# Kernel optimization log

Hardware: AMD Instinct MI355X
Metric: run time of the kernel (lower is better)

## Reference

```python
import jax, jax.numpy as jnp
import numpy as np

K = 3          # kernel_size (hardcoded in forward)
D = 1          # dilation (hardcoded in forward)
ALPHA_3 = 1.0  # self.alpha_3
THRESH = 0.1   # self.vetorch_thresh


def unfold_wo_center(x):
    """x: (B, C, H, W) -> neighbors (B, C, K*K-1, H, W), center excluded.
    Matches F.unfold(kernel=K, dilation=D, padding same) reshaped to
    (B, C, K*K, H, W) with the center tap (index K*K//2) removed.
    Implemented as shifted views of the zero-padded input (no im2col blowup
    beyond the necessary K*K-1 copies)."""
    B, C, H, W = x.shape
    pad = (K + (D - 1) * (K - 1)) // 2
    xp = jnp.pad(x, ((0, 0), (0, 0), (pad, pad), (pad, pad)))
    offs = [(i * D, j * D) for i in range(K) for j in range(K)]
    del offs[(K * K) // 2]  # drop center -> 8 neighbors for K=3
    nbrs = jnp.stack([xp[:, :, oy:oy + H, ox:ox + W] for oy, ox in offs], axis=2)
    return nbrs  # (B, C, 8, H, W)


def _neighbor_norm(x):
    # ||x_p - x_q||_2 over channel dim -> (B, 8, H, W)
    diff = x[:, :, None] - unfold_wo_center(x)
    return jnp.sqrt(jnp.sum(diff * diff, axis=1))


def setup_inputs() -> dict:
    key = jax.random.key(0)
    k1, k2 = jax.random.split(key)
    return {
        "images_lab": jax.random.normal(k1, (16, 3, 256, 256), dtype=jnp.float32),
        "pixel_vector": jax.random.normal(k2, (16, 6, 256, 256), dtype=jnp.float32),
    }


def reference(images_lab, pixel_vector):
    # get_lab_neighbor_diff: exp(-alpha * ||lab diff||)
    W_ij = jnp.exp(-ALPHA_3 * _neighbor_norm(images_lab))   # (B, 8, H, W)
    # get_vector_neighbor_diff: ||embedding diff||
    vector_ij = _neighbor_norm(pixel_vector)                # (B, 8, H, W)
    # neighbor_loss = mean((W_ij >= thresh) * vector_ij)
    neighbor_loss = jnp.mean(
        (W_ij >= THRESH).astype(vector_ij.dtype) * vector_ij
    )
    sim_maps = jnp.concatenate([W_ij, vector_ij], axis=1)   # (B, 16, H, W)
    return sim_maps, neighbor_loss
```

## Files before the change

### kernel.cpp

```cpp
#include <hip/hip_runtime.h>

#define HWSZ 65536
#define OUT_MAPS (16 * 16 * HWSZ)
#define NBLK 512

typedef float fvec4 __attribute__((ext_vector_type(4)));

__device__ __forceinline__ void expand_row(fvec4 m, int lane, float v[6]) {
    float lft = __shfl_up(m.w, 1, 64);
    float rgt = __shfl_down(m.x, 1, 64);
    if (lane == 0)  lft = 0.f;
    if (lane == 63) rgt = 0.f;
    v[0] = lft; v[1] = m.x; v[2] = m.y; v[3] = m.z; v[4] = m.w; v[5] = rgt;
}

__global__ __launch_bounds__(256, 2) void sim_main(
    const float* __restrict__ lab,
    const float* __restrict__ vec,
    float* __restrict__ out,
    float* __restrict__ partials)
{
    const int bs   = ((blockIdx.x & 7) << 6) | (blockIdx.x >> 3);
    const int g    = bs * 256 + threadIdx.x;
    const int lane = threadIdx.x & 63;
    const int wv   = g >> 6;
    const int b    = wv >> 7;
    const int h0   = (wv & 127) << 1;
    const int w0   = lane << 2;

    const bool hasU = (h0 > 0);
    const bool hasD = (h0 < 254);

    constexpr int DY[8] = {-1,-1,-1, 0, 0, 1, 1, 1};
    constexpr int DX[8] = {-1, 0, 1,-1, 1,-1, 0, 1};

    const fvec4 zz = {0.f, 0.f, 0.f, 0.f};

    fvec4 L[3][4];
    fvec4 V[6][4];
    {
        const float* pl = lab + b * 3 * HWSZ + h0 * 256 + w0;
        #pragma unroll
        for (int c = 0; c < 3; ++c) {
            L[c][0] = hasU ? *reinterpret_cast<const fvec4*>(pl + c * HWSZ - 256) : zz;
            L[c][1] =        *reinterpret_cast<const fvec4*>(pl + c * HWSZ);
            L[c][2] =        *reinterpret_cast<const fvec4*>(pl + c * HWSZ + 256);
            L[c][3] = hasD ? *reinterpret_cast<const fvec4*>(pl + c * HWSZ + 512) : zz;
        }
        const float* pv = vec + b * 6 * HWSZ + h0 * 256 + w0;
        #pragma unroll
        for (int c = 0; c < 6; ++c) {
            V[c][0] = hasU ? *reinterpret_cast<const fvec4*>(pv + c * HWSZ - 256) : zz;
            V[c][1] =        *reinterpret_cast<const fvec4*>(pv + c * HWSZ);
            V[c][2] =        *reinterpret_cast<const fvec4*>(pv + c * HWSZ + 256);
            V[c][3] = hasD ? *reinterpret_cast<const fvec4*>(pv + c * HWSZ + 512) : zz;
        }
    }

    float accA[8][4], accB[8][4];
    float* ob = out + b * 16 * HWSZ + h0 * 256 + w0;

    #pragma unroll
    for (int k = 0; k < 8; ++k)
        #pragma unroll
        for (int j = 0; j < 4; ++j) { accA[k][j] = 0.f; accB[k][j] = 0.f; }

    #pragma unroll
    for (int c = 0; c < 3; ++c) {
        float v[4][6];
        #pragma unroll
        for (int r = 0; r < 4; ++r) expand_row(L[c][r], lane, v[r]);
        #pragma unroll
        for (int k = 0; k < 8; ++k) {
            const int r = DY[k] + 1, dx = DX[k];
            #pragma unroll
            for (int j = 0; j < 4; ++j) {
                const float dA = v[1][j + 1] - v[r][j + 1 + dx];
                accA[k][j] = fmaf(dA, dA, accA[k][j]);
                const float dB = v[2][j + 1] - v[r + 1][j + 1 + dx];
                accB[k][j] = fmaf(dB, dB, accB[k][j]);
            }
        }
    }

    unsigned maskA = 0, maskB = 0;
    #pragma unroll
    for (int k = 0; k < 8; ++k) {
        float wA[4], wB[4];
        #pragma unroll
        for (int j = 0; j < 4; ++j) {
            wA[j] = __expf(-__builtin_amdgcn_sqrtf(accA[k][j]));
            wB[j] = __expf(-__builtin_amdgcn_sqrtf(accB[k][j]));
            if (wA[j] >= 0.1f) maskA |= 1u << (k * 4 + j);
            if (wB[j] >= 0.1f) maskB |= 1u << (k * 4 + j);
        }
        fvec4 sA = {wA[0], wA[1], wA[2], wA[3]};
        fvec4 sB = {wB[0], wB[1], wB[2], wB[3]};
        *reinterpret_cast<fvec4*>(ob + k * HWSZ)       = sA;
        *reinterpret_cast<fvec4*>(ob + k * HWSZ + 256) = sB;
    }

    #pragma unroll
    for (int k = 0; k < 8; ++k)
        #pragma unroll
        for (int j = 0; j < 4; ++j) { accA[k][j] = 0.f; accB[k][j] = 0.f; }

    #pragma unroll
    for (int c = 0; c < 6; ++c) {
        float v[4][6];
        #pragma unroll
        for (int r = 0; r < 4; ++r) expand_row(V[c][r], lane, v[r]);
        #pragma unroll
        for (int k = 0; k < 8; ++k) {
            const int r = DY[k] + 1, dx = DX[k];
            #pragma unroll
            for (int j = 0; j < 4; ++j) {
                const float dA = v[1][j + 1] - v[r][j + 1 + dx];
                accA[k][j] = fmaf(dA, dA, accA[k][j]);
                const float dB = v[2][j + 1] - v[r + 1][j + 1 + dx];
                accB[k][j] = fmaf(dB, dB, accB[k][j]);
            }
        }
    }

    float lsum = 0.f;
    #pragma unroll
    for (int k = 0; k < 8; ++k) {
        float vA[4], vB[4];
        #pragma unroll
        for (int j = 0; j < 4; ++j) {
            vA[j] = __builtin_amdgcn_sqrtf(accA[k][j]);
            vB[j] = __builtin_amdgcn_sqrtf(accB[k][j]);
            if (maskA & (1u << (k * 4 + j))) lsum += vA[j];
            if (maskB & (1u << (k * 4 + j))) lsum += vB[j];
        }
        fvec4 sA = {vA[0], vA[1], vA[2], vA[3]};
        fvec4 sB = {vB[0], vB[1], vB[2], vB[3]};
        *reinterpret_cast<fvec4*>(ob + (8 + k) * HWSZ)       = sA;
        *reinterpret_cast<fvec4*>(ob + (8 + k) * HWSZ + 256) = sB;
    }

    #pragma unroll
    for (int off = 32; off > 0; off >>= 1)
        lsum += __shfl_down(lsum, off, 64);
    __shared__ float ws[4];
    const int wid = threadIdx.x >> 6;
    if (lane == 0) ws[wid] = lsum;
    __syncthreads();
    if (threadIdx.x == 0)
        partials[blockIdx.x] = ws[0] + ws[1] + ws[2] + ws[3];
}

__global__ __launch_bounds__(256) void loss_reduce(
    const float* __restrict__ partials, float* __restrict__ out_loss)
{
    float s = 0.f;
    #pragma unroll
    for (int i = 0; i < NBLK / 256; ++i)
        s += partials[i * 256 + threadIdx.x];
    #pragma unroll
    for (int off = 32; off > 0; off >>= 1)
        s += __shfl_down(s, off, 64);
    __shared__ float ws[4];
    const int lane = threadIdx.x & 63;
    const int wid  = threadIdx.x >> 6;
    if (lane == 0) ws[wid] = s;
    __syncthreads();
    if (threadIdx.x == 0)
        out_loss[0] = (ws[0] + ws[1] + ws[2] + ws[3]) / 8388608.0f;
}

extern "C" void kernel_launch(void* const* d_in, const int* in_sizes, int n_in,
                              void* d_out, int out_size, void* d_ws, size_t ws_size,
                              hipStream_t stream) {
    const float* lab = (const float*)d_in[0];
    const float* vec = (const float*)d_in[1];
    float* out      = (float*)d_out;
    float* partials = (float*)d_ws;

    sim_main<<<NBLK, 256, 0, stream>>>(lab, vec, out, partials);
    loss_reduce<<<1, 256, 0, stream>>>(partials, out + OUT_MAPS);
}
```

Before: 23.46 us.

## Process four rows per wave to reuse halo rows and defer loads

Each wave now produces four output rows instead of two. Its input window grows from four rows to six, so the halo overhead per output row drops (about 1.5x reads instead of 2x). Blocks shrink to 128 threads so the grid size stays the same. The last two input rows are loaded only after the first half's compute is issued, which overlaps that memory latency with ALU work. The cost is higher register pressure and half as many waves in flight, which can reduce latency hiding in a kernel that is mostly memory-bound.

```diff
diff --git a/kernel.cpp b/kernel.cpp
--- a/kernel.cpp
+++ b/kernel.cpp
@@ -14,73 +14,84 @@
     v[0] = lft; v[1] = m.x; v[2] = m.y; v[3] = m.z; v[4] = m.w; v[5] = rgt;
 }
 
-__global__ __launch_bounds__(256, 2) void sim_main(
+__device__ __forceinline__ void stencil2(const float v[4][6],
+                                         float accA[8][4], float accB[8][4]) {
+    constexpr int DY[8] = {-1,-1,-1, 0, 0, 1, 1, 1};
+    constexpr int DX[8] = {-1, 0, 1,-1, 1,-1, 0, 1};
+    #pragma unroll
+    for (int k = 0; k < 8; ++k) {
+        const int r = DY[k] + 1, dx = DX[k];
+        #pragma unroll
+        for (int j = 0; j < 4; ++j) {
+            const float dA = v[1][j + 1] - v[r][j + 1 + dx];
+            accA[k][j] = fmaf(dA, dA, accA[k][j]);
+            const float dB = v[2][j + 1] - v[r + 1][j + 1 + dx];
+            accB[k][j] = fmaf(dB, dB, accB[k][j]);
+        }
+    }
+}
+
+__global__ __launch_bounds__(128, 2) void sim_main(
     const float* __restrict__ lab,
     const float* __restrict__ vec,
     float* __restrict__ out,
     float* __restrict__ partials)
 {
     const int bs   = ((blockIdx.x & 7) << 6) | (blockIdx.x >> 3);
-    const int g    = bs * 256 + threadIdx.x;
     const int lane = threadIdx.x & 63;
-    const int wv   = g >> 6;
-    const int b    = wv >> 7;
-    const int h0   = (wv & 127) << 1;
+    const int wid  = threadIdx.x >> 6;
+    const int wv   = bs * 2 + wid;
+    const int b    = wv >> 6;
+    const int h0   = (wv & 63) << 2;
     const int w0   = lane << 2;
 
     const bool hasU = (h0 > 0);
-    const bool hasD = (h0 < 254);
-
-    constexpr int DY[8] = {-1,-1,-1, 0, 0, 1, 1, 1};
-    constexpr int DX[8] = {-1, 0, 1,-1, 1,-1, 0, 1};
+    const bool hasD = (h0 < 252);
 
     const fvec4 zz = {0.f, 0.f, 0.f, 0.f};
-
-    fvec4 L[3][4];
-    fvec4 V[6][4];
-    {
-        const float* pl = lab + b * 3 * HWSZ + h0 * 256 + w0;
-        #pragma unroll
-        for (int c = 0; c < 3; ++c) {
-            L[c][0] = hasU ? *reinterpret_cast<const fvec4*>(pl + c * HWSZ - 256) : zz;
-            L[c][1] =        *reinterpret_cast<const fvec4*>(pl + c * HWSZ);
-            L[c][2] =        *reinterpret_cast<const fvec4*>(pl + c * HWSZ + 256);
-            L[c][3] = hasD ? *reinterpret_cast<const fvec4*>(pl + c * HWSZ + 512) : zz;
-        }
-        const float* pv = vec + b * 6 * HWSZ + h0 * 256 + w0;
-        #pragma unroll
-        for (int c = 0; c < 6; ++c) {
-            V[c][0] = hasU ? *reinterpret_cast<const fvec4*>(pv + c * HWSZ - 256) : zz;
-            V[c][1] =        *reinterpret_cast<const fvec4*>(pv + c * HWSZ);
-            V[c][2] =        *reinterpret_cast<const fvec4*>(pv + c * HWSZ + 256);
-            V[c][3] = hasD ? *reinterpret_cast<const fvec4*>(pv + c * HWSZ + 512) : zz;
-        }
+    const float* pl = lab + b * 3 * HWSZ + h0 * 256 + w0;
+    const float* pv = vec + b * 6 * HWSZ + h0 * 256 + w0;
+    float* ob = out + b * 16 * HWSZ + h0 * 256 + w0;
+
+    fvec4 L0[3], L1[3], L2[3], L3[3], L4[3], L5[3];
+    fvec4 V0[6], V1[6], V2[6], V3[6], V4[6], V5[6];
+    #pragma unroll
+    for (int c = 0; c < 3; ++c) {
+        L0[c] = hasU ? *reinterpret_cast<const fvec4*>(pl + c * HWSZ - 256) : zz;
+        L1[c] =        *reinterpret_cast<const fvec4*>(pl + c * HWSZ);
+        L2[c] =        *reinterpret_cast<const fvec4*>(pl + c * HWSZ + 256);
+        L3[c] =        *reinterpret_cast<const fvec4*>(pl + c * HWSZ + 512);
+    }
+    #pragma unroll
+    for (int c = 0; c < 6; ++c) {
+        V0[c] = hasU ? *reinterpret_cast<const fvec4*>(pv + c * HWSZ - 256) : zz;
+        V1[c] =        *reinterpret_cast<const fvec4*>(pv + c * HWSZ);
+        V2[c] =        *reinterpret_cast<const fvec4*>(pv + c * HWSZ + 256);
+        V3[c] =        *reinterpret_cast<const fvec4*>(pv + c * HWSZ + 512);
     }
 
     float accA[8][4], accB[8][4];
-    float* ob = out + b * 16 * HWSZ + h0 * 256 + w0;
-
-    #pragma unroll
-    for (int k = 0; k < 8; ++k)
-        #pragma unroll
-        for (int j = 0; j < 4; ++j) { accA[k][j] = 0.f; accB[k][j] = 0.f; }
-
-    #pragma unroll
-    for (int c = 0; c < 3; ++c) {
-        float v[4][6];
-        #pragma unroll
-        for (int r = 0; r < 4; ++r) expand_row(L[c][r], lane, v[r]);
-        #pragma unroll
-        for (int k = 0; k < 8; ++k) {
-            const int r = DY[k] + 1, dx = DX[k];
-            #pragma unroll
-            for (int j = 0; j < 4; ++j) {
-                const float dA = v[1][j + 1] - v[r][j + 1 + dx];
-                accA[k][j] = fmaf(dA, dA, accA[k][j]);
-                const float dB = v[2][j + 1] - v[r + 1][j + 1 + dx];
-                accB[k][j] = fmaf(dB, dB, accB[k][j]);
-            }
-        }
+    float lsum = 0.f;
+
+    #pragma unroll
+    for (int k = 0; k < 8; ++k)
+        #pragma unroll
+        for (int j = 0; j < 4; ++j) { accA[k][j] = 0.f; accB[k][j] = 0.f; }
+
+    #pragma unroll
+    for (int c = 0; c < 3; ++c) {
+        float v[4][6];
+        expand_row(L0[c], lane, v[0]);
+        expand_row(L1[c], lane, v[1]);
+        expand_row(L2[c], lane, v[2]);
+        expand_row(L3[c], lane, v[3]);
+        stencil2(v, accA, accB);
+    }
+
+    #pragma unroll
+    for (int c = 0; c < 3; ++c) {
+        L4[c] =        *reinterpret_cast<const fvec4*>(pl + c * HWSZ + 768);
+        L5[c] = hasD ? *reinterpret_cast<const fvec4*>(pl + c * HWSZ + 1024) : zz;
     }
 
     unsigned maskA = 0, maskB = 0;
@@ -108,22 +119,19 @@
     #pragma unroll
     for (int c = 0; c < 6; ++c) {
         float v[4][6];
-        #pragma unroll
-        for (int r = 0; r < 4; ++r) expand_row(V[c][r], lane, v[r]);
-        #pragma unroll
-        for (int k = 0; k < 8; ++k) {
-            const int r = DY[k] + 1, dx = DX[k];
-            #pragma unroll
-            for (int j = 0; j < 4; ++j) {
-                const float dA = v[1][j + 1] - v[r][j + 1 + dx];
-                accA[k][j] = fmaf(dA, dA, accA[k][j]);
-                const float dB = v[2][j + 1] - v[r + 1][j + 1 + dx];
-                accB[k][j] = fmaf(dB, dB, accB[k][j]);
-            }
-        }
-    }
-
-    float lsum = 0.f;
+        expand_row(V0[c], lane, v[0]);
+        expand_row(V1[c], lane, v[1]);
+        expand_row(V2[c], lane, v[2]);
+        expand_row(V3[c], lane, v[3]);
+        stencil2(v, accA, accB);
+    }
+
+    #pragma unroll
+    for (int c = 0; c < 6; ++c) {
+        V4[c] =        *reinterpret_cast<const fvec4*>(pv + c * HWSZ + 768);
+        V5[c] = hasD ? *reinterpret_cast<const fvec4*>(pv + c * HWSZ + 1024) : zz;
+    }
+
     #pragma unroll
     for (int k = 0; k < 8; ++k) {
         float vA[4], vB[4];
@@ -141,14 +149,76 @@
     }
 
     #pragma unroll
+    for (int k = 0; k < 8; ++k)
+        #pragma unroll
+        for (int j = 0; j < 4; ++j) { accA[k][j] = 0.f; accB[k][j] = 0.f; }
+
+    #pragma unroll
+    for (int c = 0; c < 3; ++c) {
+        float v[4][6];
+        expand_row(L2[c], lane, v[0]);
+        expand_row(L3[c], lane, v[1]);
+        expand_row(L4[c], lane, v[2]);
+        expand_row(L5[c], lane, v[3]);
+        stencil2(v, accA, accB);
+    }
+
+    maskA = 0; maskB = 0;
+    #pragma unroll
+    for (int k = 0; k < 8; ++k) {
+        float wA[4], wB[4];
+        #pragma unroll
+        for (int j = 0; j < 4; ++j) {
+            wA[j] = __expf(-__builtin_amdgcn_sqrtf(accA[k][j]));
+            wB[j] = __expf(-__builtin_amdgcn_sqrtf(accB[k][j]));
+            if (wA[j] >= 0.1f) maskA |= 1u << (k * 4 + j);
+            if (wB[j] >= 0.1f) maskB |= 1u << (k * 4 + j);
+        }
+        fvec4 sA = {wA[0], wA[1], wA[2], wA[3]};
+        fvec4 sB = {wB[0], wB[1], wB[2], wB[3]};
+        *reinterpret_cast<fvec4*>(ob + k * HWSZ + 512) = sA;
+        *reinterpret_cast<fvec4*>(ob + k * HWSZ + 768) = sB;
+    }
+
+    #pragma unroll
+    for (int k = 0; k < 8; ++k)
+        #pragma unroll
+        for (int j = 0; j < 4; ++j) { accA[k][j] = 0.f; accB[k][j] = 0.f; }
+
+    #pragma unroll
+    for (int c = 0; c < 6; ++c) {
+        float v[4][6];
+        expand_row(V2[c], lane, v[0]);
+        expand_row(V3[c], lane, v[1]);
+        expand_row(V4[c], lane, v[2]);
+        expand_row(V5[c], lane, v[3]);
+        stencil2(v, accA, accB);
+    }
+
+    #pragma unroll
+    for (int k = 0; k < 8; ++k) {
+        float vA[4], vB[4];
+        #pragma unroll
+        for (int j = 0; j < 4; ++j) {
+            vA[j] = __builtin_amdgcn_sqrtf(accA[k][j]);
+            vB[j] = __builtin_amdgcn_sqrtf(accB[k][j]);
+            if (maskA & (1u << (k * 4 + j))) lsum += vA[j];
+            if (maskB & (1u << (k * 4 + j))) lsum += vB[j];
+        }
+        fvec4 sA = {vA[0], vA[1], vA[2], vA[3]};
+        fvec4 sB = {vB[0], vB[1], vB[2], vB[3]};
+        *reinterpret_cast<fvec4*>(ob + (8 + k) * HWSZ + 512) = sA;
+        *reinterpret_cast<fvec4*>(ob + (8 + k) * HWSZ + 768) = sB;
+    }
+
+    #pragma unroll
     for (int off = 32; off > 0; off >>= 1)
         lsum += __shfl_down(lsum, off, 64);
-    __shared__ float ws[4];
-    const int wid = threadIdx.x >> 6;
+    __shared__ float ws[2];
     if (lane == 0) ws[wid] = lsum;
     __syncthreads();
     if (threadIdx.x == 0)
-        partials[blockIdx.x] = ws[0] + ws[1] + ws[2] + ws[3];
+        partials[blockIdx.x] = ws[0] + ws[1];
 }
 
 __global__ __launch_bounds__(256) void loss_reduce(
@@ -178,6 +248,6 @@
     float* out      = (float*)d_out;
     float* partials = (float*)d_ws;
 
-    sim_main<<<NBLK, 256, 0, stream>>>(lab, vec, out, partials);
+    sim_main<<<NBLK, 128, 0, stream>>>(lab, vec, out, partials);
     loss_reduce<<<1, 256, 0, stream>>>(partials, out + OUT_MAPS);
 }
```

Result: slower. 38.58 us (+64.4%).
